# Kernel optimization log

Measured on AMD Instinct MI355X. Metric: run time of the kernel, lower is better.

The kernel has to match this reference:

```python
import jax, jax.numpy as jnp
import numpy as np

B, N, H, W = 4, 256, 256, 256  # N == H required by the original code's view()

def setup_inputs() -> dict:
    key = jax.random.key(0)
    k1, k2, k3, k4, k5 = jax.random.split(key, 5)
    predictions = jax.random.normal(k1, (B, H, W), dtype=jnp.float32)
    # exactly one center per (b, n) channel
    cr = jax.random.randint(k2, (B, N), 0, H)
    cc = jax.random.randint(k3, (B, N), 0, W)
    bi = jnp.arange(B)[:, None] * jnp.ones((1, N), jnp.int32)
    ni = jnp.arange(N)[None, :] * jnp.ones((B, 1), jnp.int32)
    target_centers = jnp.zeros((B, N, H, W), jnp.int32).at[bi, ni, cr, cc].set(1)
    targets = jax.random.randint(k4, (B, N, H, W), 0, 2).astype(jnp.int32)
    pad_mask = jax.random.randint(k5, (B, N), 0, 2).astype(jnp.bool_)
    return {"predictions": predictions, "target_centers": target_centers,
            "targets": targets, "pad_mask": pad_mask}

def reference(predictions, target_centers, targets, pad_mask):
    b, n, h, w = targets.shape
    # extract the (unique) center coordinate of each channel (replaces torch.where)
    flat_idx = jnp.argmax(target_centers.reshape(b, n, h * w), axis=-1)  # [B,N]
    center_rows = flat_idx // w
    center_cols = flat_idx % w
    rows = jnp.arange(h, dtype=jnp.int32)[:, None]   # [H,1]
    cols = jnp.arange(w, dtype=jnp.int32)[None, :]   # [1,W]
    # broadcast per-pixel squared distance to each channel's center: [B,N,H,W]
    squared_dist = ((rows[None, None] - center_rows[:, :, None, None]) ** 2
                    + (cols[None, None] - center_cols[:, :, None, None]) ** 2)
    pixel_importance = targets.astype(jnp.float32) / (squared_dist.astype(jnp.float32) + 1e-6)
    pixel_importance = jnp.where(pad_mask[:, :, None, None], 0.0, pixel_importance)
    pixel_importance = pixel_importance.sum(axis=1)  # [B,H,W]
    tsum = targets.sum(axis=1)                        # int, [B,H,W]
    importance_coeff = jnp.invert(tsum).astype(jnp.float32) * 0.5  # torch ~int semantics
    pixel_importance = pixel_importance + importance_coeff
    z = tsum.astype(jnp.float32)
    x = predictions
    # BCE with logits, stable form (matches F.binary_cross_entropy_with_logits)
    bce = jnp.maximum(x, 0.0) - x * z + jnp.log1p(jnp.exp(-jnp.abs(x)))
    return jnp.mean(bce * pixel_importance)
```

## Files before the change

### kernel.cpp

```cpp
#include <hip/hip_runtime.h>
#include <stdint.h>

#define BATCH 4
#define NCH   256
#define HH    256
#define WW    256
#define HWSZ  (HH * WW)
#define NPIX  (BATCH * HWSZ)

__global__ __launch_bounds__(256) void find_centers(
    const int* __restrict__ tc, int* __restrict__ centers)
{
    __shared__ int wsum[4];
    const int bn  = blockIdx.x;
    const int tid = threadIdx.x;
    const int4* p = (const int4*)(tc + (size_t)bn * HWSZ);

    int acc = 0;
    #pragma unroll 8
    for (int i = 0; i < HWSZ / 4 / 256; ++i) {
        const int idx = i * 256 + tid;
        const int4 v = p[idx];
        const int b4 = idx * 4;
        acc += v.x * b4 + v.y * (b4 + 1) + v.z * (b4 + 2) + v.w * (b4 + 3);
    }

    #pragma unroll
    for (int o = 32; o > 0; o >>= 1) acc += __shfl_down(acc, o, 64);
    if ((tid & 63) == 0) wsum[tid >> 6] = acc;
    __syncthreads();
    if (tid == 0) centers[bn] = wsum[0] + wsum[1] + wsum[2] + wsum[3];
}

__global__ __launch_bounds__(256) void loss_kernel(
    const float* __restrict__ pred,
    const int*   __restrict__ targets,
    const unsigned char* __restrict__ padraw,
    const int*   __restrict__ centers,
    float*       __restrict__ out)
{
    __shared__ float2 cinfo[NCH];
    __shared__ int    modeflag;
    __shared__ float  wsum[4];

    const int tid = threadIdx.x;
    if (tid == 0) modeflag = 0;
    __syncthreads();

    {
        const unsigned int wv = ((const unsigned int*)padraw)[tid];
        if (wv & 0xFFFFFF00u) modeflag = 1;
    }
    __syncthreads();

    const int b    = blockIdx.x >> 8;
    const int hrow = blockIdx.x & 255;

    {
        const int n    = tid;
        const int cidx = centers[b * NCH + n];
        const int cr   = cidx >> 8;
        const int cc   = cidx & 255;
        int pad;
        if (modeflag) pad = (padraw[b * NCH + n] != 0);
        else          pad = (((const int*)padraw)[b * NCH + n] != 0);
        const int dh = hrow - cr;
        float fdh2e = (float)(dh * dh) + 1e-6f;
        if (pad) fdh2e = __builtin_inff();
        cinfo[n] = make_float2(fdh2e, (float)cc);
    }
    __syncthreads();

    const float wcolf = (float)tid;
    const int* base = targets + (size_t)b * NCH * HWSZ + hrow * WW + tid;

    int   tsum = 0;
    float imp  = 0.f;

    #pragma unroll 16
    for (int n = 0; n < NCH; ++n) {
        const int    v = base[(size_t)n * HWSZ];
        const float2 c = cinfo[n];
        const float fdw = wcolf - c.y;
        const float f   = __builtin_fmaf(fdw, fdw, c.x);
        imp = __builtin_fmaf((float)v, __builtin_amdgcn_rcpf(f), imp);
        tsum += v;
    }

    const float it = __builtin_fmaf((float)(~tsum), 0.5f, imp);

    const float x   = pred[b * HWSZ + hrow * WW + tid];
    const float bce = fmaxf(x, 0.f) - x * (float)tsum + log1pf(expf(-fabsf(x)));

    float contrib = bce * it;

    #pragma unroll
    for (int o = 32; o > 0; o >>= 1) contrib += __shfl_down(contrib, o, 64);
    const int wave = tid >> 6;
    if ((tid & 63) == 0) wsum[wave] = contrib;
    __syncthreads();
    if (tid == 0) {
        const float s = wsum[0] + wsum[1] + wsum[2] + wsum[3];
        atomicAdd(out, s * (1.0f / (float)NPIX));
    }
}

extern "C" void kernel_launch(void* const* d_in, const int* in_sizes, int n_in,
                              void* d_out, int out_size, void* d_ws, size_t ws_size,
                              hipStream_t stream)
{
    const float* pred = (const float*)d_in[0];
    const int*   tc   = (const int*)d_in[1];
    const int*   tg   = (const int*)d_in[2];
    const unsigned char* pm = (const unsigned char*)d_in[3];
    float* out   = (float*)d_out;
    int* centers = (int*)d_ws;

    hipMemsetAsync(d_out, 0, sizeof(float), stream);
    find_centers<<<BATCH * NCH, 256, 0, stream>>>(tc, centers);
    loss_kernel<<<BATCH * HH, 256, 0, stream>>>(pred, tg, pm, centers, out);
}
```

Before: 507.4 us.

## Vectorize loss kernel to int4 loads with single-wave blocks

Each loss block now runs one 64-lane wave instead of 256 threads, and each thread handles four adjacent columns, reading targets and predictions as int4/float4. The shared-memory mode flag and the cross-wave reduction are replaced by a wave ballot and a single shuffle reduction, which removes two barriers. The aim is wider memory transactions and less sync overhead on the bandwidth-bound pass over targets. The cost is only 64 threads per block with more registers each, which may reduce latency hiding on the strided per-channel loads.

```diff
diff --git a/kernel.cpp b/kernel.cpp
--- a/kernel.cpp
+++ b/kernel.cpp
@@ -32,7 +32,7 @@
     if (tid == 0) centers[bn] = wsum[0] + wsum[1] + wsum[2] + wsum[3];
 }
 
-__global__ __launch_bounds__(256) void loss_kernel(
+__global__ __launch_bounds__(64) void loss_kernel(
     const float* __restrict__ pred,
     const int*   __restrict__ targets,
     const unsigned char* __restrict__ padraw,
@@ -40,30 +40,28 @@
     float*       __restrict__ out)
 {
     __shared__ float2 cinfo[NCH];
-    __shared__ int    modeflag;
-    __shared__ float  wsum[4];
 
-    const int tid = threadIdx.x;
-    if (tid == 0) modeflag = 0;
-    __syncthreads();
-
-    {
-        const unsigned int wv = ((const unsigned int*)padraw)[tid];
-        if (wv & 0xFFFFFF00u) modeflag = 1;
-    }
-    __syncthreads();
-
+    const int tid  = threadIdx.x;
     const int b    = blockIdx.x >> 8;
     const int hrow = blockIdx.x & 255;
 
-    {
-        const int n    = tid;
+    bool upper = false;
+    #pragma unroll
+    for (int k = 0; k < 4; ++k) {
+        const unsigned int wv = ((const unsigned int*)padraw)[tid + 64 * k];
+        upper = upper || ((wv & 0xFFFFFF00u) != 0u);
+    }
+    const bool u8mode = (__ballot(upper) != 0ull);
+
+    #pragma unroll
+    for (int k = 0; k < 4; ++k) {
+        const int n    = tid + 64 * k;
         const int cidx = centers[b * NCH + n];
         const int cr   = cidx >> 8;
         const int cc   = cidx & 255;
         int pad;
-        if (modeflag) pad = (padraw[b * NCH + n] != 0);
-        else          pad = (((const int*)padraw)[b * NCH + n] != 0);
+        if (u8mode) pad = (padraw[b * NCH + n] != 0);
+        else        pad = (((const int*)padraw)[b * NCH + n] != 0);
         const int dh = hrow - cr;
         float fdh2e = (float)(dh * dh) + 1e-6f;
         if (pad) fdh2e = __builtin_inff();
@@ -71,38 +69,50 @@
     }
     __syncthreads();
 
-    const float wcolf = (float)tid;
-    const int* base = targets + (size_t)b * NCH * HWSZ + hrow * WW + tid;
+    const int4* base =
+        (const int4*)(targets + (size_t)b * NCH * HWSZ + hrow * WW) + tid;
+    const float w0 = (float)(tid * 4);
 
-    int   tsum = 0;
-    float imp  = 0.f;
+    int   ts0 = 0, ts1 = 0, ts2 = 0, ts3 = 0;
+    float im0 = 0.f, im1 = 0.f, im2 = 0.f, im3 = 0.f;
 
     #pragma unroll 16
     for (int n = 0; n < NCH; ++n) {
-        const int    v = base[(size_t)n * HWSZ];
+        const int4   v = base[n * (HWSZ / 4)];
         const float2 c = cinfo[n];
-        const float fdw = wcolf - c.y;
-        const float f   = __builtin_fmaf(fdw, fdw, c.x);
-        imp = __builtin_fmaf((float)v, __builtin_amdgcn_rcpf(f), imp);
-        tsum += v;
+        const float d0 = w0 - c.y;
+        const float d1 = d0 + 1.0f;
+        const float d2 = d0 + 2.0f;
+        const float d3 = d0 + 3.0f;
+        im0 = __builtin_fmaf((float)v.x,
+              __builtin_amdgcn_rcpf(__builtin_fmaf(d0, d0, c.x)), im0);
+        im1 = __builtin_fmaf((float)v.y,
+              __builtin_amdgcn_rcpf(__builtin_fmaf(d1, d1, c.x)), im1);
+        im2 = __builtin_fmaf((float)v.z,
+              __builtin_amdgcn_rcpf(__builtin_fmaf(d2, d2, c.x)), im2);
+        im3 = __builtin_fmaf((float)v.w,
+              __builtin_amdgcn_rcpf(__builtin_fmaf(d3, d3, c.x)), im3);
+        ts0 += v.x; ts1 += v.y; ts2 += v.z; ts3 += v.w;
     }
 
-    const float it = __builtin_fmaf((float)(~tsum), 0.5f, imp);
+    const float4 xv =
+        *(const float4*)(pred + (size_t)b * HWSZ + hrow * WW + tid * 4);
 
-    const float x   = pred[b * HWSZ + hrow * WW + tid];
-    const float bce = fmaxf(x, 0.f) - x * (float)tsum + log1pf(expf(-fabsf(x)));
+    const float it0 = __builtin_fmaf((float)(~ts0), 0.5f, im0);
+    const float it1 = __builtin_fmaf((float)(~ts1), 0.5f, im1);
+    const float it2 = __builtin_fmaf((float)(~ts2), 0.5f, im2);
+    const float it3 = __builtin_fmaf((float)(~ts3), 0.5f, im3);
 
-    float contrib = bce * it;
+    const float bce0 = fmaxf(xv.x, 0.f) - xv.x * (float)ts0 + log1pf(expf(-fabsf(xv.x)));
+    const float bce1 = fmaxf(xv.y, 0.f) - xv.y * (float)ts1 + log1pf(expf(-fabsf(xv.y)));
+    const float bce2 = fmaxf(xv.z, 0.f) - xv.z * (float)ts2 + log1pf(expf(-fabsf(xv.z)));
+    const float bce3 = fmaxf(xv.w, 0.f) - xv.w * (float)ts3 + log1pf(expf(-fabsf(xv.w)));
+
+    float contrib = bce0 * it0 + bce1 * it1 + bce2 * it2 + bce3 * it3;
 
     #pragma unroll
     for (int o = 32; o > 0; o >>= 1) contrib += __shfl_down(contrib, o, 64);
-    const int wave = tid >> 6;
-    if ((tid & 63) == 0) wsum[wave] = contrib;
-    __syncthreads();
-    if (tid == 0) {
-        const float s = wsum[0] + wsum[1] + wsum[2] + wsum[3];
-        atomicAdd(out, s * (1.0f / (float)NPIX));
-    }
+    if (tid == 0) atomicAdd(out, contrib * (1.0f / (float)NPIX));
 }
 
 extern "C" void kernel_launch(void* const* d_in, const int* in_sizes, int n_in,
@@ -118,5 +128,5 @@
 
     hipMemsetAsync(d_out, 0, sizeof(float), stream);
     find_centers<<<BATCH * NCH, 256, 0, stream>>>(tc, centers);
-    loss_kernel<<<BATCH * HH, 256, 0, stream>>>(pred, tg, pm, centers, out);
+    loss_kernel<<<BATCH * HH, 64, 0, stream>>>(pred, tg, pm, centers, out);
 }
```

Measured after the change: 512.2 us. About the same (+1.0%).
